# Optimization experiments

Hardware: AMD Instinct MI355X
Metric: run time of the kernel (lower is better)

Reference implementation:

```python
import jax, jax.numpy as jnp
import numpy as np

N_NODES = 150000  # n_users + m_items
NUM_LAYERS = 3


def setup_inputs() -> dict:
    key = jax.random.key(0)
    k1, k2 = jax.random.split(key)
    x = jax.random.normal(k1, (N_NODES, 64), dtype=jnp.float32) * 0.1
    edge_index = jax.random.randint(k2, (2, 4800000), 0, N_NODES, dtype=jnp.int64)
    return {"x": x, "edge_index": edge_index}


def _lightgcn_propagate(x, row, col, deg_inv_sqrt):
    # message: norm * x[row], aggregated into col (sum)
    norm = deg_inv_sqrt[row] * deg_inv_sqrt[col]  # [E]
    msg = x[row] * norm[:, None]                   # [E, D]
    return jax.ops.segment_sum(msg, col, num_segments=x.shape[0])


def reference(x, edge_index):
    row, col = edge_index[0], edge_index[1]
    # symmetric GCN normalization: deg from destination nodes
    ones = jnp.ones(row.shape, dtype=x.dtype)
    deg = jax.ops.segment_sum(ones, col, num_segments=x.shape[0])
    deg_inv_sqrt = jnp.where(deg > 0, jax.lax.rsqrt(jnp.maximum(deg, 1.0)), 0.0)

    alpha = 1.0 / (1.0 + NUM_LAYERS)
    out = jnp.zeros_like(x)
    h = x
    for _ in range(NUM_LAYERS):
        h = _lightgcn_propagate(h, row, col, deg_inv_sqrt)
        out = out + alpha * h
    return out
```

## Files before the change

kernel.cpp:

```cpp
#include <hip/hip_runtime.h>
#include <hip/hip_fp16.h>
#include <math.h>

#define N_NODES 150000
#define D 64
#define NEDGE 4800000
#define NUM_LAYERS 3

#define BSHIFT 8
#define NBUCKET ((N_NODES + 255) >> 8)
#define NBPAD 768
#define BINTILE 8192
#define NBIN_BLOCKS ((NEDGE + BINTILE - 1) / BINTILE)
#define SCAP 9216

typedef float v2f __attribute__((ext_vector_type(2)));

__global__ void hist_bucket(const int4* __restrict__ col4, int* __restrict__ bcount) {
    __shared__ int h[NBUCKET];
    for (int i = threadIdx.x; i < NBUCKET; i += blockDim.x) h[i] = 0;
    __syncthreads();
    int i = blockIdx.x * blockDim.x + threadIdx.x;
    int stride = gridDim.x * blockDim.x;
    for (int e = i; e < NEDGE / 4; e += stride) {
        int4 c = col4[e];
        atomicAdd(&h[c.x >> BSHIFT], 1);
        atomicAdd(&h[c.y >> BSHIFT], 1);
        atomicAdd(&h[c.z >> BSHIFT], 1);
        atomicAdd(&h[c.w >> BSHIFT], 1);
    }
    __syncthreads();
    for (int b = threadIdx.x; b < NBUCKET; b += blockDim.x)
        if (h[b]) atomicAdd(&bcount[b], h[b]);
}

__global__ void scan_buckets(const int* __restrict__ bcount, int* __restrict__ bbase,
                             int* __restrict__ bcur16, int* __restrict__ off) {
    __shared__ int tsum[256];
    int t = threadIdx.x;
    int loc[3];
    int s = 0;
#pragma unroll
    for (int k = 0; k < 3; k++) {
        int idx = t * 3 + k;
        int x = (idx < NBUCKET) ? bcount[idx] : 0;
        loc[k] = x;
        s += x;
    }
    tsum[t] = s;
    __syncthreads();
    for (int ofs = 1; ofs < 256; ofs <<= 1) {
        int xv = (t >= ofs) ? tsum[t - ofs] : 0;
        __syncthreads();
        tsum[t] += xv;
        __syncthreads();
    }
    int run = (t > 0) ? tsum[t - 1] : 0;
#pragma unroll
    for (int k = 0; k < 3; k++) {
        int idx = t * 3 + k;
        if (idx < NBUCKET) bbase[idx] = run;
        bcur16[idx * 16] = run;
        run += loc[k];
    }
    if (t == 255) {
        bbase[NBUCKET] = NEDGE;
        off[N_NODES] = NEDGE;
    }
}

__global__ void __launch_bounds__(256) binpass2(const int* __restrict__ row,
                                                const int* __restrict__ col,
                                                int* __restrict__ bcur16,
                                                unsigned* __restrict__ bin) {
    __shared__ unsigned srec[BINTILE];
    __shared__ int hist[NBPAD];
    __shared__ int lscan[NBPAD];
    __shared__ int lcur[NBPAD];
    __shared__ int gbase[NBPAD];
    __shared__ int tsum[256];
    int t = threadIdx.x;
    int base = blockIdx.x * BINTILE;
    int n = NEDGE - base;
    if (n > BINTILE) n = BINTILE;
    for (int i = t; i < NBPAD; i += 256) hist[i] = 0;
    __syncthreads();
    for (int i = t; i < n; i += 256)
        atomicAdd(&hist[col[base + i] >> BSHIFT], 1);
    __syncthreads();
    int b0 = t * 3;
    int l0 = hist[b0], l1 = hist[b0 + 1], l2 = hist[b0 + 2];
    tsum[t] = l0 + l1 + l2;
    __syncthreads();
    for (int ofs = 1; ofs < 256; ofs <<= 1) {
        int xv = (t >= ofs) ? tsum[t - ofs] : 0;
        __syncthreads();
        tsum[t] += xv;
        __syncthreads();
    }
    int run = (t > 0) ? tsum[t - 1] : 0;
    lscan[b0] = run; lcur[b0] = run;
    lscan[b0 + 1] = run + l0; lcur[b0 + 1] = run + l0;
    lscan[b0 + 2] = run + l0 + l1; lcur[b0 + 2] = run + l0 + l1;
    gbase[b0]     = l0 ? atomicAdd(&bcur16[b0 * 16], l0) : 0;
    gbase[b0 + 1] = l1 ? atomicAdd(&bcur16[(b0 + 1) * 16], l1) : 0;
    gbase[b0 + 2] = l2 ? atomicAdd(&bcur16[(b0 + 2) * 16], l2) : 0;
    __syncthreads();
    for (int i = t; i < n; i += 256) {
        int c = col[base + i];
        int r = row[base + i];
        int b = c >> BSHIFT;
        int pos = atomicAdd(&lcur[b], 1);
        srec[pos] = (unsigned)r | ((unsigned)(c & 255) << 18);
    }
    __syncthreads();
#pragma unroll
    for (int k = 0; k < 3; k++) {
        int b = b0 + k;
        int s = lscan[b], e2 = lcur[b], gb = gbase[b];
        for (int j = s; j < e2; j++) bin[gb + (j - s)] = srec[j];
    }
}

__global__ void __launch_bounds__(256) sortpass2(const unsigned* __restrict__ bin,
                                                 const int* __restrict__ bbase,
                                                 float* __restrict__ dis,
                                                 int* __restrict__ off,
                                                 unsigned* __restrict__ ewf) {
    __shared__ unsigned srec[SCAP];
    __shared__ int hist[256];
    __shared__ int sc[256];
    __shared__ int ncur[256];
    int b = blockIdx.x, t = threadIdx.x;
    int s = bbase[b], e = bbase[b + 1];
    int len = e - s;
    int nst = len < SCAP ? len : SCAP;
    for (int i = t; i < nst; i += 256) srec[i] = bin[s + i];
    hist[t] = 0;
    __syncthreads();
    for (int i = t; i < nst; i += 256)
        atomicAdd(&hist[srec[i] >> 18], 1);
    for (int i = nst + t; i < len; i += 256)
        atomicAdd(&hist[bin[s + i] >> 18], 1);
    __syncthreads();
    int val = hist[t];
    sc[t] = val;
    __syncthreads();
    for (int ofs = 1; ofs < 256; ofs <<= 1) {
        int xv = (t >= ofs) ? sc[t - ofs] : 0;
        __syncthreads();
        sc[t] += xv;
        __syncthreads();
    }
    int ex = sc[t] - val;
    ncur[t] = ex;
    int node = (b << BSHIFT) + t;
    if (node < N_NODES) {
        dis[node] = (val > 0) ? (1.0f / sqrtf((float)val)) : 0.0f;
        off[node] = s + ex;
    }
    __syncthreads();
    for (int i = t; i < nst; i += 256) {
        unsigned rec = srec[i];
        int c = (int)(rec >> 18);
        int pos = s + atomicAdd(&ncur[c], 1);
        ewf[pos] = rec & 0x3FFFFu;
    }
    for (int i = nst + t; i < len; i += 256) {
        unsigned rec = bin[s + i];
        int c = (int)(rec >> 18);
        int pos = s + atomicAdd(&ncur[c], 1);
        ewf[pos] = rec & 0x3FFFFu;
    }
}

__global__ void cvt_g0(const float4* __restrict__ x4, const float* __restrict__ dis,
                       uint2* __restrict__ g0) {
    int i = blockIdx.x * blockDim.x + threadIdx.x;
    if (i >= N_NODES * 16) return;
    float w = dis[i >> 4];
    float4 v = x4[i];
    __half2 a = __floats2half2_rn(w * v.x, w * v.y);
    __half2 b = __floats2half2_rn(w * v.z, w * v.w);
    uint2 r;
    r.x = *reinterpret_cast<unsigned*>(&a);
    r.y = *reinterpret_cast<unsigned*>(&b);
    g0[i] = r;
}

template <bool FINAL>
__global__ void layer8(const char* __restrict__ hbase, const int* __restrict__ off,
                       const unsigned* __restrict__ ewf, const float* __restrict__ dis,
                       char* __restrict__ hout, const char* __restrict__ hA,
                       const char* __restrict__ hB, float4* __restrict__ out4,
                       float alpha) {
    int wid = (blockIdx.x * blockDim.x + threadIdx.x) >> 6;
    if (wid >= N_NODES) return;
    unsigned lane = threadIdx.x & 63u;
    unsigned g = lane >> 3;
    unsigned sub16 = (lane & 7u) << 4;
    int s = off[wid], e = off[wid + 1];
    v2f acc[4];
#pragma unroll
    for (int k = 0; k < 4; k++) acc[k] = (v2f){0.f, 0.f};

    auto ACC = [&](uint4 v) {
        const __half2* p = reinterpret_cast<const __half2*>(&v);
#pragma unroll
        for (int k = 0; k < 4; k++) {
            float2 f = __half22float2(p[k]);
            acc[k] += (v2f){f.x, f.y};
        }
    };
    auto ROW = [&](unsigned r) {
        return *reinterpret_cast<const uint4*>(hbase + ((r << 7) | sub16));
    };

    int i = s + (int)g;
    for (; i + 24 < e; i += 32) {
        unsigned r0 = ewf[i], r1 = ewf[i + 8], r2 = ewf[i + 16], r3 = ewf[i + 24];
        uint4 v0 = ROW(r0), v1 = ROW(r1), v2 = ROW(r2), v3 = ROW(r3);
        ACC(v0); ACC(v1); ACC(v2); ACC(v3);
    }
    for (; i < e; i += 8) ACC(ROW(ewf[i]));

#pragma unroll
    for (int m = 8; m <= 32; m <<= 1)
#pragma unroll
        for (int k = 0; k < 4; k++) {
            acc[k].x += __shfl_xor(acc[k].x, m, 64);
            acc[k].y += __shfl_xor(acc[k].y, m, 64);
        }

    if (g != 0) return;
    float w = dis[wid];
    unsigned ro = ((unsigned)wid << 7) | sub16;
    if (FINAL) {
        float inv = (w > 0.f) ? 1.0f / w : 0.f;
        uint4 a = *reinterpret_cast<const uint4*>(hA + ro);
        uint4 b = *reinterpret_cast<const uint4*>(hB + ro);
        const __half2* pa = reinterpret_cast<const __half2*>(&a);
        const __half2* pb = reinterpret_cast<const __half2*>(&b);
        float r[8];
#pragma unroll
        for (int k = 0; k < 4; k++) {
            float2 fa = __half22float2(pa[k]);
            float2 fb = __half22float2(pb[k]);
            r[2 * k]     = alpha * (inv * (fa.x + fb.x) + w * acc[k].x);
            r[2 * k + 1] = alpha * (inv * (fa.y + fb.y) + w * acc[k].y);
        }
        unsigned sub = (lane & 7u);
        out4[(size_t)wid * 16 + sub * 2]     = make_float4(r[0], r[1], r[2], r[3]);
        out4[(size_t)wid * 16 + sub * 2 + 1] = make_float4(r[4], r[5], r[6], r[7]);
    } else {
        float w2 = w * w;
        __half2 q[4];
#pragma unroll
        for (int k = 0; k < 4; k++)
            q[k] = __floats2half2_rn(w2 * acc[k].x, w2 * acc[k].y);
        uint4 st;
        st.x = *reinterpret_cast<unsigned*>(&q[0]);
        st.y = *reinterpret_cast<unsigned*>(&q[1]);
        st.z = *reinterpret_cast<unsigned*>(&q[2]);
        st.w = *reinterpret_cast<unsigned*>(&q[3]);
        *reinterpret_cast<uint4*>(hout + ro) = st;
    }
}

extern "C" void kernel_launch(void* const* d_in, const int* in_sizes, int n_in,
                              void* d_out, int out_size, void* d_ws, size_t ws_size,
                              hipStream_t stream) {
    const float* x = (const float*)d_in[0];
    const int* edges = (const int*)d_in[1];
    const int* row = edges;
    const int* col = edges + NEDGE;
    float4* out4 = (float4*)d_out;

    char* ws = (char*)d_ws;
    size_t p = 0;
    auto alloc = [&](size_t bytes) {
        void* r = ws + p;
        p += (bytes + 255) & ~(size_t)255;
        return r;
    };
    int* bcount = (int*)alloc((size_t)NBUCKET * 4);
    int* bbase = (int*)alloc((size_t)(NBUCKET + 1) * 4);
    int* bcur16 = (int*)alloc((size_t)NBPAD * 16 * 4);
    float* dis = (float*)alloc((size_t)N_NODES * 4);
    int* off = (int*)alloc((size_t)(N_NODES + 1) * 4);
    unsigned* ewf = (unsigned*)alloc((size_t)NEDGE * 4);
    char* g0 = (char*)alloc((size_t)N_NODES * D * 2);
    char* region = (char*)alloc((size_t)N_NODES * D * 2);
    unsigned* bin = (unsigned*)region;
    char* g1 = region;
    char* g2 = (char*)alloc((size_t)N_NODES * D * 2);

    hipMemsetAsync(bcount, 0, (size_t)NBUCKET * 4, stream);
    hist_bucket<<<512, 256, 0, stream>>>((const int4*)col, bcount);
    scan_buckets<<<1, 256, 0, stream>>>(bcount, bbase, bcur16, off);
    binpass2<<<NBIN_BLOCKS, 256, 0, stream>>>(row, col, bcur16, bin);
    sortpass2<<<NBUCKET, 256, 0, stream>>>(bin, bbase, dis, off, ewf);
    cvt_g0<<<(N_NODES * 16 + 255) / 256, 256, 0, stream>>>((const float4*)x, dis,
                                                           (uint2*)g0);

    const float alpha = 1.0f / (1.0f + NUM_LAYERS);
    int grid = (N_NODES * 64 + 255) / 256;
    layer8<false><<<grid, 256, 0, stream>>>(g0, off, ewf, dis,
                                            g1, nullptr, nullptr, nullptr, alpha);
    layer8<false><<<grid, 256, 0, stream>>>(g1, off, ewf, dis,
                                            g2, nullptr, nullptr, nullptr, alpha);
    layer8<true><<<grid, 256, 0, stream>>>(g2, off, ewf, dis,
                                           nullptr, g1, g2, out4, alpha);
}
```

Measured before the change: 385.2 us.

## Use contiguous edge chunks per lane group, fma_mix accumulation, nontemporal stores

Each 8-lane group in the gather kernel now handles a contiguous chunk of the node's edge list instead of a stride-8 interleave. The fp16-to-fp32 convert-and-add is replaced with inline v_fma_mix_f32 instructions. Output and intermediate stores become nontemporal. The aim is fewer instructions in the accumulation loop and less cache pollution from the stores. The risks are uneven chunk lengths across groups for low-degree nodes, less coalesced index loads within a wave, and an unchanged fixed summation order apart from the chunking.

```diff
diff --git a/kernel.cpp b/kernel.cpp
--- a/kernel.cpp
+++ b/kernel.cpp
@@ -14,7 +14,8 @@
 #define NBIN_BLOCKS ((NEDGE + BINTILE - 1) / BINTILE)
 #define SCAP 9216
 
-typedef float v2f __attribute__((ext_vector_type(2)));
+typedef float vf4 __attribute__((ext_vector_type(4)));
+typedef unsigned vu4 __attribute__((ext_vector_type(4)));
 
 __global__ void hist_bucket(const int4* __restrict__ col4, int* __restrict__ bcount) {
     __shared__ int h[NBUCKET];
@@ -192,7 +193,7 @@
 __global__ void layer8(const char* __restrict__ hbase, const int* __restrict__ off,
                        const unsigned* __restrict__ ewf, const float* __restrict__ dis,
                        char* __restrict__ hout, const char* __restrict__ hA,
-                       const char* __restrict__ hB, float4* __restrict__ out4,
+                       const char* __restrict__ hB, float* __restrict__ outf,
                        float alpha) {
     int wid = (blockIdx.x * blockDim.x + threadIdx.x) >> 6;
     if (wid >= N_NODES) return;
@@ -200,37 +201,53 @@
     unsigned g = lane >> 3;
     unsigned sub16 = (lane & 7u) << 4;
     int s = off[wid], e = off[wid + 1];
-    v2f acc[4];
-#pragma unroll
-    for (int k = 0; k < 4; k++) acc[k] = (v2f){0.f, 0.f};
-
-    auto ACC = [&](uint4 v) {
-        const __half2* p = reinterpret_cast<const __half2*>(&v);
-#pragma unroll
-        for (int k = 0; k < 4; k++) {
-            float2 f = __half22float2(p[k]);
-            acc[k] += (v2f){f.x, f.y};
-        }
-    };
+    int L = (e - s + 7) >> 3;
+    int cs = s + (int)g * L;
+    int ce = cs + L;
+    if (ce > e) ce = e;
+
+    float a0 = 0.f, a1 = 0.f, a2 = 0.f, a3 = 0.f;
+    float a4 = 0.f, a5 = 0.f, a6 = 0.f, a7 = 0.f;
+
     auto ROW = [&](unsigned r) {
         return *reinterpret_cast<const uint4*>(hbase + ((r << 7) | sub16));
     };
-
-    int i = s + (int)g;
-    for (; i + 24 < e; i += 32) {
-        unsigned r0 = ewf[i], r1 = ewf[i + 8], r2 = ewf[i + 16], r3 = ewf[i + 24];
+#define ACCD(d, aL, aH)                                                          \
+    asm("v_fma_mix_f32 %0, %2, 1.0, %0 op_sel:[0,0,0] op_sel_hi:[1,0,0]\n\t"     \
+        "v_fma_mix_f32 %1, %2, 1.0, %1 op_sel:[1,0,0] op_sel_hi:[1,0,0]"         \
+        : "+v"(aL), "+v"(aH) : "v"(d))
+#define ACCV(v)                \
+    do {                       \
+        ACCD((v).x, a0, a1);   \
+        ACCD((v).y, a2, a3);   \
+        ACCD((v).z, a4, a5);   \
+        ACCD((v).w, a6, a7);   \
+    } while (0)
+
+    int i = cs;
+    for (; i + 3 < ce; i += 4) {
+        unsigned r0 = ewf[i], r1 = ewf[i + 1], r2 = ewf[i + 2], r3 = ewf[i + 3];
         uint4 v0 = ROW(r0), v1 = ROW(r1), v2 = ROW(r2), v3 = ROW(r3);
-        ACC(v0); ACC(v1); ACC(v2); ACC(v3);
-    }
-    for (; i < e; i += 8) ACC(ROW(ewf[i]));
+        ACCV(v0); ACCV(v1); ACCV(v2); ACCV(v3);
+    }
+    for (; i < ce; ++i) {
+        uint4 v = ROW(ewf[i]);
+        ACCV(v);
+    }
+#undef ACCV
+#undef ACCD
 
 #pragma unroll
-    for (int m = 8; m <= 32; m <<= 1)
-#pragma unroll
-        for (int k = 0; k < 4; k++) {
-            acc[k].x += __shfl_xor(acc[k].x, m, 64);
-            acc[k].y += __shfl_xor(acc[k].y, m, 64);
-        }
+    for (int m = 8; m <= 32; m <<= 1) {
+        a0 += __shfl_xor(a0, m, 64);
+        a1 += __shfl_xor(a1, m, 64);
+        a2 += __shfl_xor(a2, m, 64);
+        a3 += __shfl_xor(a3, m, 64);
+        a4 += __shfl_xor(a4, m, 64);
+        a5 += __shfl_xor(a5, m, 64);
+        a6 += __shfl_xor(a6, m, 64);
+        a7 += __shfl_xor(a7, m, 64);
+    }
 
     if (g != 0) return;
     float w = dis[wid];
@@ -241,29 +258,34 @@
         uint4 b = *reinterpret_cast<const uint4*>(hB + ro);
         const __half2* pa = reinterpret_cast<const __half2*>(&a);
         const __half2* pb = reinterpret_cast<const __half2*>(&b);
-        float r[8];
-#pragma unroll
-        for (int k = 0; k < 4; k++) {
-            float2 fa = __half22float2(pa[k]);
-            float2 fb = __half22float2(pb[k]);
-            r[2 * k]     = alpha * (inv * (fa.x + fb.x) + w * acc[k].x);
-            r[2 * k + 1] = alpha * (inv * (fa.y + fb.y) + w * acc[k].y);
-        }
+        float2 f0 = __half22float2(pa[0]), f1 = __half22float2(pa[1]);
+        float2 f2 = __half22float2(pa[2]), f3 = __half22float2(pa[3]);
+        float2 q0 = __half22float2(pb[0]), q1 = __half22float2(pb[1]);
+        float2 q2 = __half22float2(pb[2]), q3 = __half22float2(pb[3]);
+        vf4 o0 = {alpha * (inv * (f0.x + q0.x) + w * a0),
+                  alpha * (inv * (f0.y + q0.y) + w * a1),
+                  alpha * (inv * (f1.x + q1.x) + w * a2),
+                  alpha * (inv * (f1.y + q1.y) + w * a3)};
+        vf4 o1 = {alpha * (inv * (f2.x + q2.x) + w * a4),
+                  alpha * (inv * (f2.y + q2.y) + w * a5),
+                  alpha * (inv * (f3.x + q3.x) + w * a6),
+                  alpha * (inv * (f3.y + q3.y) + w * a7)};
         unsigned sub = (lane & 7u);
-        out4[(size_t)wid * 16 + sub * 2]     = make_float4(r[0], r[1], r[2], r[3]);
-        out4[(size_t)wid * 16 + sub * 2 + 1] = make_float4(r[4], r[5], r[6], r[7]);
+        vf4* dst = reinterpret_cast<vf4*>(outf + (size_t)wid * 64 + sub * 8);
+        __builtin_nontemporal_store(o0, dst);
+        __builtin_nontemporal_store(o1, dst + 1);
     } else {
         float w2 = w * w;
-        __half2 q[4];
-#pragma unroll
-        for (int k = 0; k < 4; k++)
-            q[k] = __floats2half2_rn(w2 * acc[k].x, w2 * acc[k].y);
-        uint4 st;
-        st.x = *reinterpret_cast<unsigned*>(&q[0]);
-        st.y = *reinterpret_cast<unsigned*>(&q[1]);
-        st.z = *reinterpret_cast<unsigned*>(&q[2]);
-        st.w = *reinterpret_cast<unsigned*>(&q[3]);
-        *reinterpret_cast<uint4*>(hout + ro) = st;
+        __half2 q0 = __floats2half2_rn(w2 * a0, w2 * a1);
+        __half2 q1 = __floats2half2_rn(w2 * a2, w2 * a3);
+        __half2 q2 = __floats2half2_rn(w2 * a4, w2 * a5);
+        __half2 q3 = __floats2half2_rn(w2 * a6, w2 * a7);
+        vu4 st;
+        st.x = *reinterpret_cast<unsigned*>(&q0);
+        st.y = *reinterpret_cast<unsigned*>(&q1);
+        st.z = *reinterpret_cast<unsigned*>(&q2);
+        st.w = *reinterpret_cast<unsigned*>(&q3);
+        __builtin_nontemporal_store(st, reinterpret_cast<vu4*>(hout + ro));
     }
 }
 
@@ -274,7 +296,7 @@
     const int* edges = (const int*)d_in[1];
     const int* row = edges;
     const int* col = edges + NEDGE;
-    float4* out4 = (float4*)d_out;
+    float* outf = (float*)d_out;
 
     char* ws = (char*)d_ws;
     size_t p = 0;
@@ -310,5 +332,5 @@
     layer8<false><<<grid, 256, 0, stream>>>(g1, off, ewf, dis,
                                             g2, nullptr, nullptr, nullptr, alpha);
     layer8<true><<<grid, 256, 0, stream>>>(g2, off, ewf, dis,
-                                           nullptr, g1, g2, out4, alpha);
-}
+                                           nullptr, g1, g2, outf, alpha);
+}
```

Result: no change. 380.1 us (-1.3%).
